# Kernel tuning notes

Measured on AMD Instinct MI355X. Metric: run time of the kernel, lower is better.

The kernel has to match this reference:

```python
import jax, jax.numpy as jnp
import numpy as np

K, D = 2048, 256
B, H, W = 16, 64, 64
DECAY = 0.99
EPS = 1e-05


def setup_inputs() -> dict:
    key = jax.random.key(0)
    k1, k2, k3 = jax.random.split(key, 3)
    z_e = jax.random.normal(k1, (B, D, H, W), dtype=jnp.float32)
    codebook = jax.random.normal(k2, (K, D), dtype=jnp.float32)
    ema_count = jnp.zeros((K,), dtype=jnp.float32)
    ema_weight = jax.random.normal(k3, (K, D), dtype=jnp.float32)
    return {"z_e": z_e, "codebook": codebook, "ema_count": ema_count, "ema_weight": ema_weight}


def reference(z_e, codebook, ema_count, ema_weight):
    b, d, h, w = z_e.shape
    k = codebook.shape[0]
    # [B, D, H, W] -> [B*H*W, D]
    flat = jnp.transpose(z_e, (0, 2, 3, 1)).reshape(-1, d)
    # squared euclidean distances to each code: [N, K]
    dist = (jnp.sum(flat * flat, axis=1, keepdims=True)
            - 2.0 * (flat @ codebook.T)
            + jnp.sum(codebook * codebook, axis=1))
    idx = jnp.argmin(dist, axis=1)  # [N] int
    # gather nearest codes -> [B, D, H, W]
    z_q = jnp.transpose(codebook[idx].reshape(b, h, w, d), (0, 3, 1, 2))
    # EMA statistics (training path, no_grad in torch)
    n = jax.ops.segment_sum(jnp.ones_like(idx, dtype=flat.dtype), idx, num_segments=k)  # [K]
    dw = jax.ops.segment_sum(flat, idx, num_segments=k)  # [K, D]
    new_ema_count = ema_count * DECAY + (1.0 - DECAY) * n
    new_ema_weight = ema_weight * DECAY + (1.0 - DECAY) * dw
    new_codebook = new_ema_weight / (new_ema_count + EPS)[:, None]
    # commitment loss and straight-through estimator
    loss_commit = jnp.mean(jnp.square(z_e - z_q))
    z_q_st = z_e + jax.lax.stop_gradient(z_q - z_e)
    return (z_q_st, idx.reshape(b, h, w), loss_commit,
            new_codebook, new_ema_count, new_ema_weight)
```

## Files before the change

kernel.cpp:

```cpp
#include <hip/hip_runtime.h>
#include <hip/hip_bf16.h>


#define KC 2048
#define DD 256
#define NB 16
#define HWS 4096
#define NPTS 65536
#define DECAYF 0.99f
#define ONEMD 0.01f
#define EPSF 1e-5f
#define NCH 2
#define MARGIN 0.0625f
#define CHPTS 64
#define FPT 64
#define NLOSS 4096

typedef __attribute__((ext_vector_type(8))) short short8v;
typedef __attribute__((ext_vector_type(16))) float f32x16;

#define WS_IDX     0
#define WS_SORTED  262144
#define WS_CNTI    524288
#define WS_START   532480
#define WS_CURSOR  540672
#define WS_FLAGCNT 548864
#define WS_FLAGS   549120
#define WS_LOSSP   549120
#define WS_CNORM   811264
#define WS_PART    819456
#define WS_CBH     5013760
#define WS_CBL     6062336
#define WS_ZH      7110912
#define WS_ZL      40665344
#define WS_NEED_MFMA 74219776ULL
#define WS_NEED_MID  5013760ULL

#define OUT_ZQ   0
#define OUT_IDX  16777216
#define OUT_LOSS (OUT_IDX + NPTS)
#define OUT_CB   (OUT_LOSS + 1)
#define OUT_CNT  (OUT_CB + KC*DD)
#define OUT_W    (OUT_CNT + KC)

static __device__ __forceinline__ unsigned short f2bf_rn(float x) {
    unsigned u = __builtin_bit_cast(unsigned, x);
    unsigned r = (u + 0x7FFFu + ((u >> 16) & 1u)) >> 16;
    return (unsigned short)r;
}
static __device__ __forceinline__ float bf2f(unsigned short h) {
    unsigned u = ((unsigned)h) << 16;
    return __builtin_bit_cast(float, u);
}
static __device__ __forceinline__ void gload_lds16(const unsigned short* g,
                                                   unsigned short* l) {
    __builtin_amdgcn_global_load_lds(
        (const __attribute__((address_space(1))) void*)g,
        (__attribute__((address_space(3))) void*)l, 16, 0, 0);
}

__global__ __launch_bounds__(256) void cbsplit_kernel(const float* __restrict__ cb,
                                                      float* __restrict__ cnorm,
                                                      unsigned short* __restrict__ cbs_h,
                                                      unsigned short* __restrict__ cbs_l) {
    int k = blockIdx.x * 256 + threadIdx.x;
    if (k >= KC) return;
    const int ct = k >> 5, lc = k & 31;
    const float4* row = reinterpret_cast<const float4*>(cb + (size_t)k * DD);
    float s = 0.f;
    #pragma unroll 4
    for (int chunk = 0; chunk < 32; ++chunk) {
        float4 v0 = row[chunk * 2], v1 = row[chunk * 2 + 1];
        float v[8] = {v0.x, v0.y, v0.z, v0.w, v1.x, v1.y, v1.z, v1.w};
        unsigned short hh[8], ll[8];
        #pragma unroll
        for (int j = 0; j < 8; ++j) {
            s += v[j] * v[j];
            hh[j] = f2bf_rn(v[j]);
            ll[j] = f2bf_rn(v[j] - bf2f(hh[j]));
        }
        const int ks = chunk >> 1, h = chunk & 1;
        size_t dst = (size_t)ct * 8192 + ks * 512 + (h * 32 + lc) * 8;
        *reinterpret_cast<ushort4*>(cbs_h + dst)     = *(ushort4*)&hh[0];
        *reinterpret_cast<ushort4*>(cbs_h + dst + 4) = *(ushort4*)&hh[4];
        *reinterpret_cast<ushort4*>(cbs_l + dst)     = *(ushort4*)&ll[0];
        *reinterpret_cast<ushort4*>(cbs_l + dst + 4) = *(ushort4*)&ll[4];
    }
    cnorm[k] = s;
}

__global__ __launch_bounds__(256) void cnorm_kernel(const float* __restrict__ cb,
                                                    float* __restrict__ cnorm) {
    int k = blockIdx.x * 256 + threadIdx.x;
    if (k < KC) {
        const float4* row = reinterpret_cast<const float4*>(cb + (size_t)k * DD);
        float s = 0.f;
        #pragma unroll 8
        for (int i = 0; i < DD / 4; ++i) {
            float4 v = row[i];
            s += v.x * v.x + v.y * v.y + v.z * v.z + v.w * v.w;
        }
        cnorm[k] = s;
    }
}

__global__ __launch_bounds__(256) void transpose_split_kernel(const float* __restrict__ z_e,
                                                              unsigned short* __restrict__ zh,
                                                              unsigned short* __restrict__ zl) {
    __shared__ float t_lds[64][65];
    const int tid = threadIdx.x;
    const int hw0 = blockIdx.x * 64;
    const int d0 = blockIdx.y * 64;
    const int b = blockIdx.z;
    const float* src = z_e + (size_t)b * DD * HWS;
    #pragma unroll
    for (int i = 0; i < 16; ++i) {
        int li = tid + i * 256;
        int d = li >> 6, hw = li & 63;
        t_lds[d][hw] = src[(size_t)(d0 + d) * HWS + hw0 + hw];
    }
    __syncthreads();
    #pragma unroll
    for (int i = 0; i < 16; ++i) {
        int li = tid + i * 256;
        int p = li >> 6, d = li & 63;
        float x = t_lds[d][p];
        unsigned short h = f2bf_rn(x);
        unsigned short l = f2bf_rn(x - bf2f(h));
        size_t o = ((size_t)b * HWS + hw0 + p) * DD + d0 + d;
        zh[o] = h; zl[o] = l;
    }
}

__global__ __launch_bounds__(256, 2) void argmin_mfma_kernel(const unsigned short* __restrict__ zh,
                                                             const unsigned short* __restrict__ zl,
                                                             const unsigned short* __restrict__ cbs_h,
                                                             const unsigned short* __restrict__ cbs_l,
                                                             const float* __restrict__ cnorm,
                                                             int* __restrict__ idx_out,
                                                             int* __restrict__ flagcnt,
                                                             int* __restrict__ flaglist) {
    __shared__ unsigned short lds_cb[2][2][16][512];

    const int tid = threadIdx.x;
    const int w = tid >> 6, lane = tid & 63;
    const int lc = lane & 31, h = lane >> 5;
    const int p = blockIdx.x * 128 + w * 32 + lc;

    const short8v* zhp = reinterpret_cast<const short8v*>(zh + (size_t)p * DD + h * 8);
    const short8v* zlp = reinterpret_cast<const short8v*>(zl + (size_t)p * DD + h * 8);
    short8v bh[16], bl[16];
    #pragma unroll
    for (int ks = 0; ks < 16; ++ks) { bh[ks] = zhp[ks * 2]; bl[ks] = zlp[ks * 2]; }

    auto stage = [&](int ct, int buf) {
        #pragma unroll
        for (int j = 0; j < 8; ++j) {
            const int inst = w * 8 + j;
            const int part = inst >> 4;
            const int ks = inst & 15;
            const unsigned short* src =
                (part ? cbs_l : cbs_h) + (size_t)ct * 8192 + ks * 512 + lane * 8;
            gload_lds16(src, &lds_cb[buf][part][ks][0]);
        }
    };

    float bv1 = 3.4e38f, bv2 = 3.4e38f;
    int bi1 = 0;
    int cur = 0;

    stage(0, 0);
    __syncthreads();

    for (int ct = 0; ct < KC / 32; ++ct) {
        if (ct + 1 < KC / 32) stage(ct + 1, cur ^ 1);

        f32x16 a0, a1, a2;
        #pragma unroll
        for (int i = 0; i < 16; ++i) { a0[i] = 0.f; a1[i] = 0.f; a2[i] = 0.f; }
        #pragma unroll
        for (int ks = 0; ks < 16; ++ks) {
            short8v ah = *reinterpret_cast<const short8v*>(&lds_cb[cur][0][ks][lane * 8]);
            short8v al = *reinterpret_cast<const short8v*>(&lds_cb[cur][1][ks][lane * 8]);
            a0 = __builtin_amdgcn_mfma_f32_32x32x16_bf16(ah, bh[ks], a0, 0, 0, 0);
            a1 = __builtin_amdgcn_mfma_f32_32x32x16_bf16(ah, bl[ks], a1, 0, 0, 0);
            a2 = __builtin_amdgcn_mfma_f32_32x32x16_bf16(al, bh[ks], a2, 0, 0, 0);
        }
        const float* cnb = cnorm + ct * 32 + h * 4;
        #pragma unroll
        for (int g = 0; g < 4; ++g) {
            float4 cn = *reinterpret_cast<const float4*>(cnb + g * 8);
            float cna[4] = {cn.x, cn.y, cn.z, cn.w};
            #pragma unroll
            for (int q = 0; q < 4; ++q) {
                float dot = a0[g * 4 + q] + a1[g * 4 + q] + a2[g * 4 + q];
                float v = fmaf(dot, -2.0f, cna[q]);
                int k = ct * 32 + g * 8 + h * 4 + q;
                bool lt = v < bv1;
                bv2 = fminf(bv2, fmaxf(v, bv1));
                bv1 = fminf(bv1, v);
                bi1 = lt ? k : bi1;
            }
        }
        __syncthreads();
        cur ^= 1;
    }

    float ov1 = __shfl_xor(bv1, 32, 64);
    float ov2 = __shfl_xor(bv2, 32, 64);
    int   oi1 = __shfl_xor(bi1, 32, 64);
    float nv1 = fminf(bv1, ov1);
    float nv2 = fminf(fmaxf(bv1, ov1), fminf(bv2, ov2));
    int ni1 = (ov1 < bv1 || (ov1 == bv1 && oi1 < bi1)) ? oi1 : bi1;

    if (h == 0) {
        idx_out[p] = ni1;
        if (nv2 - nv1 < MARGIN) {
            int pos = atomicAdd(flagcnt, 1);
            flaglist[pos] = p;
        }
    }
}

__global__ __launch_bounds__(256) void fixup_part_kernel(const float* __restrict__ z_e,
                                                         const float* __restrict__ cb,
                                                         const float* __restrict__ cnorm,
                                                         const int* __restrict__ flagcnt,
                                                         const int* __restrict__ flaglist,
                                                         unsigned long long* __restrict__ fixmin) {
    __shared__ float As[64][FPT + 4];
    __shared__ float Bs[64][64 + 4];
    __shared__ float rv[FPT][16];
    __shared__ int   ri[FPT][16];
    __shared__ int   zo[FPT];

    const int tid = threadIdx.x;
    const int tx = tid & 15, ty = tid >> 4;
    const int tot = *flagcnt;
    const int base = blockIdx.x * FPT;
    if (base >= tot) return;
    const int cnt = min(FPT, tot - base);
    const int kt = blockIdx.y * 64;

    if (tid < FPT) {
        int n = flaglist[base + ((tid < cnt) ? tid : 0)];
        zo[tid] = (n >> 12) * DD * HWS + (n & 4095);
    }
    __syncthreads();

    float acc[4][4] = {};
    for (int dc = 0; dc < DD; dc += 64) {
        #pragma unroll
        for (int i = 0; i < 16; ++i) {
            int li = tid + i * 256;
            int d = li >> 6, pp = li & 63;
            As[d][pp] = z_e[(size_t)zo[pp] + (size_t)(dc + d) * HWS];
        }
        #pragma unroll
        for (int i = 0; i < 16; ++i) {
            int li = tid + i * 256;
            int k = li >> 6, d = li & 63;
            Bs[d][k] = cb[(size_t)(kt + k) * DD + dc + d];
        }
        __syncthreads();
        #pragma unroll
        for (int d = 0; d < 64; ++d) {
            const float4 a4 = *reinterpret_cast<const float4*>(&As[d][ty * 4]);
            const float4 b4 = *reinterpret_cast<const float4*>(&Bs[d][tx * 4]);
            const float a[4] = {a4.x, a4.y, a4.z, a4.w};
            const float bb[4] = {b4.x, b4.y, b4.z, b4.w};
            #pragma unroll
            for (int j = 0; j < 4; ++j)
                #pragma unroll
                for (int i = 0; i < 4; ++i)
                    acc[j][i] = fmaf(a[j], bb[i], acc[j][i]);
        }
        __syncthreads();
    }

    float bestv[4]; int besti[4];
    #pragma unroll
    for (int j = 0; j < 4; ++j) { bestv[j] = 3.4e38f; besti[j] = 0; }
    #pragma unroll
    for (int i = 0; i < 4; ++i) {
        int k = kt + tx * 4 + i;
        float c = cnorm[k];
        #pragma unroll
        for (int j = 0; j < 4; ++j) {
            float dist = c - 2.0f * acc[j][i];
            if (dist < bestv[j]) { bestv[j] = dist; besti[j] = k; }
        }
    }
    #pragma unroll
    for (int j = 0; j < 4; ++j) { rv[ty * 4 + j][tx] = bestv[j]; ri[ty * 4 + j][tx] = besti[j]; }
    __syncthreads();

    if (tid < cnt) {
        float bv = rv[tid][0]; int bi = ri[tid][0];
        #pragma unroll
        for (int t = 1; t < 16; ++t) {
            float v = rv[tid][t]; int i2 = ri[tid][t];
            if (v < bv || (v == bv && i2 < bi)) { bv = v; bi = i2; }
        }
        unsigned uv = __float_as_uint(bv);
        uv = (uv & 0x80000000u) ? ~uv : (uv | 0x80000000u);
        unsigned long long key = ((unsigned long long)uv << 32) | (unsigned)bi;
        atomicMin(&fixmin[base + tid], key);
    }
}

__global__ __launch_bounds__(256) void fixup_apply_kernel(const int* __restrict__ flagcnt,
                                                          const int* __restrict__ flaglist,
                                                          const unsigned long long* __restrict__ fixmin,
                                                          int* __restrict__ idx_out) {
    int f = blockIdx.x * 256 + threadIdx.x;
    if (f < *flagcnt)
        idx_out[flaglist[f]] = (int)(fixmin[f] & 0xFFFFFFFFull);
}

#define PT 64
#define KT 64
#define DC 64
__global__ __launch_bounds__(256) void argmin_kernel(const float* __restrict__ z_e,
                                                     const float* __restrict__ cb,
                                                     const float* __restrict__ cnorm,
                                                     int* __restrict__ idx_out) {
    __shared__ float As[DC][PT + 4];
    __shared__ float Bs[DC][KT + 4];
    __shared__ float rv[PT][16];
    __shared__ int   ri[PT][16];
    const int tid = threadIdx.x;
    const int tx = tid & 15, ty = tid >> 4;
    const int n0 = blockIdx.x * PT;
    const int b = n0 >> 12;
    const int hw0 = n0 & 4095;
    const float* zb = z_e + (size_t)b * DD * HWS + hw0;
    float bestv[4]; int besti[4];
    #pragma unroll
    for (int j = 0; j < 4; ++j) { bestv[j] = 3.4e38f; besti[j] = 0; }
    for (int kt = 0; kt < KC; kt += KT) {
        float acc[4][4] = {};
        for (int dc = 0; dc < DD; dc += DC) {
            #pragma unroll
            for (int i = 0; i < 16; ++i) {
                int li = tid + i * 256;
                int d = li >> 6, pp = li & 63;
                As[d][pp] = zb[(size_t)(dc + d) * HWS + pp];
            }
            #pragma unroll
            for (int i = 0; i < 16; ++i) {
                int li = tid + i * 256;
                int k = li >> 6, d = li & 63;
                Bs[d][k] = cb[(size_t)(kt + k) * DD + dc + d];
            }
            __syncthreads();
            #pragma unroll
            for (int d = 0; d < DC; ++d) {
                const float4 a4 = *reinterpret_cast<const float4*>(&As[d][ty * 4]);
                const float4 b4 = *reinterpret_cast<const float4*>(&Bs[d][tx * 4]);
                const float a[4] = {a4.x, a4.y, a4.z, a4.w};
                const float bb[4] = {b4.x, b4.y, b4.z, b4.w};
                #pragma unroll
                for (int j = 0; j < 4; ++j)
                    #pragma unroll
                    for (int i = 0; i < 4; ++i)
                        acc[j][i] = fmaf(a[j], bb[i], acc[j][i]);
            }
            __syncthreads();
        }
        #pragma unroll
        for (int i = 0; i < 4; ++i) {
            int k = kt + tx * 4 + i;
            float c = cnorm[k];
            #pragma unroll
            for (int j = 0; j < 4; ++j) {
                float dist = c - 2.0f * acc[j][i];
                if (dist < bestv[j]) { bestv[j] = dist; besti[j] = k; }
            }
        }
    }
    #pragma unroll
    for (int j = 0; j < 4; ++j) { rv[ty * 4 + j][tx] = bestv[j]; ri[ty * 4 + j][tx] = besti[j]; }
    __syncthreads();
    if (tid < PT) {
        float bv = rv[tid][0]; int bi = ri[tid][0];
        #pragma unroll
        for (int t = 1; t < 16; ++t) {
            float v = rv[tid][t]; int i2 = ri[tid][t];
            if (v < bv || (v == bv && i2 < bi)) { bv = v; bi = i2; }
        }
        idx_out[n0 + tid] = bi;
    }
}

__global__ __launch_bounds__(256) void hist_kernel(const int* __restrict__ idx,
                                                   int* __restrict__ cnti) {
    int n = blockIdx.x * 256 + threadIdx.x;
    atomicAdd(&cnti[idx[n]], 1);
}

__global__ __launch_bounds__(256) void scan_kernel(const int* __restrict__ cnt,
                                                   int* __restrict__ start,
                                                   int* __restrict__ cursor) {
    __shared__ int ps[256];
    const int t = threadIdx.x;
    int v[8], s = 0;
    #pragma unroll
    for (int j = 0; j < 8; ++j) { v[j] = cnt[t * 8 + j]; s += v[j]; }
    ps[t] = s;
    __syncthreads();
    for (int off = 1; off < 256; off <<= 1) {
        int x = (t >= off) ? ps[t - off] : 0;
        __syncthreads();
        ps[t] += x;
        __syncthreads();
    }
    int base = ps[t] - s;
    #pragma unroll
    for (int j = 0; j < 8; ++j) { start[t * 8 + j] = base; cursor[t * 8 + j] = base; base += v[j]; }
}

__global__ __launch_bounds__(256) void scatter_ids_kernel(const int* __restrict__ idx,
                                                          int* __restrict__ cursor,
                                                          int* __restrict__ sorted,
                                                          float* __restrict__ out_idxf) {
    int n = blockIdx.x * 256 + threadIdx.x;
    int k = idx[n];
    out_idxf[n] = (float)k;
    int pos = atomicAdd(&cursor[k], 1);
    sorted[pos] = n;
}

__global__ __launch_bounds__(256) void dw_chunk_kernel(const unsigned short* __restrict__ zh,
                                                       const unsigned short* __restrict__ zl,
                                                       const int* __restrict__ sorted,
                                                       const int* __restrict__ idx,
                                                       float* __restrict__ dwacc) {
    const int t = threadIdx.x;
    const int base = blockIdx.x * CHPTS;
    int kcur = idx[sorted[base]];
    float acc = 0.f;
    for (int i = 0; i < CHPTS; ++i) {
        const int n = sorted[base + i];
        const int k = idx[n];
        if (k != kcur) {
            atomicAdd(&dwacc[(size_t)kcur * DD + t], acc);
            acc = 0.f; kcur = k;
        }
        acc += bf2f(zh[(size_t)n * DD + t]) + bf2f(zl[(size_t)n * DD + t]);
    }
    atomicAdd(&dwacc[(size_t)kcur * DD + t], acc);
}

__global__ __launch_bounds__(256) void dw_direct_kernel(const float* __restrict__ z_e,
                                                        const int* __restrict__ sorted,
                                                        const int* __restrict__ start,
                                                        const int* __restrict__ cnti,
                                                        float* __restrict__ part) {
    const int k = blockIdx.x, c = blockIdx.y, t = threadIdx.x;
    const int s0 = start[k], cnt = cnti[k];
    float acc = 0.f;
    for (int p = c; p < cnt; p += NCH) {
        int n = sorted[s0 + p];
        int b = n >> 12, hw = n & 4095;
        acc += z_e[(size_t)b * DD * HWS + (size_t)t * HWS + hw];
    }
    part[((size_t)k * NCH + c) * DD + t] = acc;
}

__global__ __launch_bounds__(256) void zq_loss_kernel(const float* __restrict__ z_e,
                                                      const float* __restrict__ cb,
                                                      const int* __restrict__ idx,
                                                      float* __restrict__ out_zq,
                                                      float* __restrict__ lossp) {
    const int tid = threadIdx.x;
    const size_t base = ((size_t)blockIdx.x * 256 + tid) * 16;
    const int hw = (int)(base & 4095);
    const int d = (int)((base >> 12) & 255);
    const int b = (int)(base >> 20);
    const int n0 = b * HWS + hw;

    const int4* ip = reinterpret_cast<const int4*>(idx + n0);
    const float4* zp = reinterpret_cast<const float4*>(z_e + base);
    float4* op = reinterpret_cast<float4*>(out_zq + base);

    float ls = 0.f;
    #pragma unroll
    for (int g = 0; g < 4; ++g) {
        int4 i4 = ip[g];
        float4 z4 = zp[g];
        int kk[4] = {i4.x, i4.y, i4.z, i4.w};
        float zz[4] = {z4.x, z4.y, z4.z, z4.w};
        float o4[4];
        #pragma unroll
        for (int q = 0; q < 4; ++q) {
            float qv = cb[(size_t)kk[q] * DD + d];
            o4[q] = zz[q] + (qv - zz[q]);
            float df = zz[q] - qv;
            ls += df * df;
        }
        float4 w4; w4.x = o4[0]; w4.y = o4[1]; w4.z = o4[2]; w4.w = o4[3];
        op[g] = w4;
    }

    #pragma unroll
    for (int off = 32; off > 0; off >>= 1) ls += __shfl_down(ls, off, 64);
    __shared__ float wsum[4];
    if ((tid & 63) == 0) wsum[tid >> 6] = ls;
    __syncthreads();
    if (tid == 0) lossp[blockIdx.x] = wsum[0] + wsum[1] + wsum[2] + wsum[3];
}

__global__ __launch_bounds__(256) void finalize_dw_kernel(const float* __restrict__ ema_count,
                                                          const float* __restrict__ ema_weight,
                                                          const int* __restrict__ cnti,
                                                          const float* __restrict__ dwacc,
                                                          const float* __restrict__ lossp,
                                                          float* __restrict__ out_cb,
                                                          float* __restrict__ out_cnt,
                                                          float* __restrict__ out_w,
                                                          float* __restrict__ out_loss) {
    const int t = blockIdx.x * 256 + threadIdx.x;
    const int k = t >> 8, d = t & 255;
    const float nc = ema_count[k] * DECAYF + ONEMD * (float)cnti[k];
    const float nw = ema_weight[t] * DECAYF + ONEMD * dwacc[t];
    out_w[t] = nw;
    out_cb[t] = nw / (nc + EPSF);
    if (d == 0) out_cnt[k] = nc;

    if (blockIdx.x == 0) {
        __shared__ double sd[256];
        const int tid = threadIdx.x;
        double s = 0.0;
        for (int i = tid; i < NLOSS; i += 256) s += (double)lossp[i];
        sd[tid] = s;
        __syncthreads();
        for (int off = 128; off > 0; off >>= 1) {
            if (tid < off) sd[tid] += sd[tid + off];
            __syncthreads();
        }
        if (tid == 0) out_loss[0] = (float)(sd[0] / 16777216.0);
    }
}

__global__ __launch_bounds__(256) void finalize_part_kernel(const float* __restrict__ ema_count,
                                                            const float* __restrict__ ema_weight,
                                                            const int* __restrict__ cnti,
                                                            const float* __restrict__ part,
                                                            const float* __restrict__ lossp,
                                                            float* __restrict__ out_cb,
                                                            float* __restrict__ out_cnt,
                                                            float* __restrict__ out_w,
                                                            float* __restrict__ out_loss) {
    const int t = blockIdx.x * 256 + threadIdx.x;
    const int k = t >> 8, d = t & 255;
    float dw = 0.f;
    #pragma unroll
    for (int c = 0; c < NCH; ++c) dw += part[((size_t)k * NCH + c) * DD + d];
    const float nc = ema_count[k] * DECAYF + ONEMD * (float)cnti[k];
    const float nw = ema_weight[t] * DECAYF + ONEMD * dw;
    out_w[t] = nw;
    out_cb[t] = nw / (nc + EPSF);
    if (d == 0) out_cnt[k] = nc;

    if (blockIdx.x == 0) {
        __shared__ double sd[256];
        const int tid = threadIdx.x;
        double s = 0.0;
        for (int i = tid; i < NLOSS; i += 256) s += (double)lossp[i];
        sd[tid] = s;
        __syncthreads();
        for (int off = 128; off > 0; off >>= 1) {
            if (tid < off) sd[tid] += sd[tid + off];
            __syncthreads();
        }
        if (tid == 0) out_loss[0] = (float)(sd[0] / 16777216.0);
    }
}

extern "C" void kernel_launch(void* const* d_in, const int* in_sizes, int n_in,
                              void* d_out, int out_size, void* d_ws, size_t ws_size,
                              hipStream_t stream) {
    const float* z_e       = (const float*)d_in[0];
    const float* codebook  = (const float*)d_in[1];
    const float* ema_count = (const float*)d_in[2];
    const float* ema_weight= (const float*)d_in[3];
    float* out = (float*)d_out;
    char* ws = (char*)d_ws;

    int*   ws_idx    = (int*)(ws + WS_IDX);
    int*   ws_sorted = (int*)(ws + WS_SORTED);
    int*   ws_cnti   = (int*)(ws + WS_CNTI);
    int*   ws_start  = (int*)(ws + WS_START);
    int*   ws_cursor = (int*)(ws + WS_CURSOR);
    int*   ws_flagc  = (int*)(ws + WS_FLAGCNT);
    int*   ws_flags  = (int*)(ws + WS_FLAGS);
    float* ws_lossp  = (float*)(ws + WS_LOSSP);
    float* ws_cnorm  = (float*)(ws + WS_CNORM);
    unsigned long long* ws_fixmin = (unsigned long long*)(ws + WS_PART);
    float* ws_dwacc  = (float*)(ws + WS_PART);
    float* ws_part   = (float*)(ws + WS_PART);
    unsigned short* ws_cbh = (unsigned short*)(ws + WS_CBH);
    unsigned short* ws_cbl = (unsigned short*)(ws + WS_CBL);
    unsigned short* ws_zh  = (unsigned short*)(ws + WS_ZH);
    unsigned short* ws_zl  = (unsigned short*)(ws + WS_ZL);

    const bool mfma_path = (ws_size >= WS_NEED_MFMA);
    const bool mid_path  = (ws_size >= WS_NEED_MID);

    hipMemsetAsync(ws + WS_CNTI, 0, (size_t)(WS_FLAGCNT + 256 - WS_CNTI), stream);

    if (mfma_path) {
        hipMemsetAsync(ws + WS_PART, 0xFF, (size_t)NPTS * 8, stream);
        cbsplit_kernel<<<(KC + 255) / 256, 256, 0, stream>>>(codebook, ws_cnorm, ws_cbh, ws_cbl);
        transpose_split_kernel<<<dim3(HWS / 64, DD / 64, NB), 256, 0, stream>>>(z_e, ws_zh, ws_zl);
        argmin_mfma_kernel<<<NPTS / 128, 256, 0, stream>>>(ws_zh, ws_zl, ws_cbh, ws_cbl,
                                                           ws_cnorm, ws_idx, ws_flagc, ws_flags);
        fixup_part_kernel<<<dim3(NPTS / FPT, KC / 64), 256, 0, stream>>>(z_e, codebook, ws_cnorm,
                                                                         ws_flagc, ws_flags,
                                                                         ws_fixmin);
        fixup_apply_kernel<<<NPTS / 256, 256, 0, stream>>>(ws_flagc, ws_flags, ws_fixmin, ws_idx);
        zq_loss_kernel<<<NLOSS, 256, 0, stream>>>(z_e, codebook, ws_idx,
                                                  out + OUT_ZQ, ws_lossp);
        hist_kernel<<<NPTS / 256, 256, 0, stream>>>(ws_idx, ws_cnti);
        scan_kernel<<<1, 256, 0, stream>>>(ws_cnti, ws_start, ws_cursor);
        scatter_ids_kernel<<<NPTS / 256, 256, 0, stream>>>(ws_idx, ws_cursor, ws_sorted,
                                                           out + OUT_IDX);
        hipMemsetAsync(ws + WS_PART, 0, (size_t)KC * DD * 4, stream);
        dw_chunk_kernel<<<NPTS / CHPTS, 256, 0, stream>>>(ws_zh, ws_zl, ws_sorted,
                                                          ws_idx, ws_dwacc);
        finalize_dw_kernel<<<(KC * DD) / 256, 256, 0, stream>>>(ema_count, ema_weight,
                                                                ws_cnti, ws_dwacc, ws_lossp,
                                                                out + OUT_CB, out + OUT_CNT,
                                                                out + OUT_W, out + OUT_LOSS);
    } else if (mid_path) {
        cnorm_kernel<<<(KC + 255) / 256, 256, 0, stream>>>(codebook, ws_cnorm);
        argmin_kernel<<<NPTS / PT, 256, 0, stream>>>(z_e, codebook, ws_cnorm, ws_idx);
        zq_loss_kernel<<<NLOSS, 256, 0, stream>>>(z_e, codebook, ws_idx,
                                                  out + OUT_ZQ, ws_lossp);
        hist_kernel<<<NPTS / 256, 256, 0, stream>>>(ws_idx, ws_cnti);
        scan_kernel<<<1, 256, 0, stream>>>(ws_cnti, ws_start, ws_cursor);
        scatter_ids_kernel<<<NPTS / 256, 256, 0, stream>>>(ws_idx, ws_cursor, ws_sorted,
                                                           out + OUT_IDX);
        dw_direct_kernel<<<dim3(KC, NCH), 256, 0, stream>>>(z_e, ws_sorted,
                                                            ws_start, ws_cnti, ws_part + KC * DD);
        finalize_part_kernel<<<(KC * DD) / 256, 256, 0, stream>>>(ema_count, ema_weight,
                                                                  ws_cnti, ws_part + KC * DD,
                                                                  ws_lossp,
                                                                  out + OUT_CB, out + OUT_CNT,
                                                                  out + OUT_W, out + OUT_LOSS);
    }
}
```

Measured before the change: 449.9 us.

## Fuse prep kernels, fold histogram into argmin, replace memsets with in-kernel zeroing

Merges the codebook split and the z_e transpose/split into one prep kernel, which also zeroes the counters. The histogram moves into argmin as atomics, with fixup_apply correcting the counts for reassigned points, and the fixmin and dwacc memsets are folded into existing kernels. CHPTS is halved so the dw chunk kernel launches more blocks. The aim is fewer launches and memsets, at the cost of extra atomics in argmin and the risk of ordering bugs, for example the cursor zeroing that scan may depend on.

```diff
diff --git a/kernel.cpp b/kernel.cpp
--- a/kernel.cpp
+++ b/kernel.cpp
@@ -12,7 +12,7 @@
 #define EPSF 1e-5f
 #define NCH 2
 #define MARGIN 0.0625f
-#define CHPTS 64
+#define CHPTS 32
 #define FPT 64
 #define NLOSS 4096
 
@@ -59,34 +59,67 @@
         (__attribute__((address_space(3))) void*)l, 16, 0, 0);
 }
 
-__global__ __launch_bounds__(256) void cbsplit_kernel(const float* __restrict__ cb,
-                                                      float* __restrict__ cnorm,
-                                                      unsigned short* __restrict__ cbs_h,
-                                                      unsigned short* __restrict__ cbs_l) {
-    int k = blockIdx.x * 256 + threadIdx.x;
-    if (k >= KC) return;
-    const int ct = k >> 5, lc = k & 31;
-    const float4* row = reinterpret_cast<const float4*>(cb + (size_t)k * DD);
-    float s = 0.f;
-    #pragma unroll 4
-    for (int chunk = 0; chunk < 32; ++chunk) {
-        float4 v0 = row[chunk * 2], v1 = row[chunk * 2 + 1];
-        float v[8] = {v0.x, v0.y, v0.z, v0.w, v1.x, v1.y, v1.z, v1.w};
-        unsigned short hh[8], ll[8];
-        #pragma unroll
-        for (int j = 0; j < 8; ++j) {
-            s += v[j] * v[j];
-            hh[j] = f2bf_rn(v[j]);
-            ll[j] = f2bf_rn(v[j] - bf2f(hh[j]));
-        }
-        const int ks = chunk >> 1, h = chunk & 1;
-        size_t dst = (size_t)ct * 8192 + ks * 512 + (h * 32 + lc) * 8;
-        *reinterpret_cast<ushort4*>(cbs_h + dst)     = *(ushort4*)&hh[0];
-        *reinterpret_cast<ushort4*>(cbs_h + dst + 4) = *(ushort4*)&hh[4];
-        *reinterpret_cast<ushort4*>(cbs_l + dst)     = *(ushort4*)&ll[0];
-        *reinterpret_cast<ushort4*>(cbs_l + dst + 4) = *(ushort4*)&ll[4];
-    }
-    cnorm[k] = s;
+__global__ __launch_bounds__(256) void prep_kernel(const float* __restrict__ z_e,
+                                                   const float* __restrict__ cb,
+                                                   float* __restrict__ cnorm,
+                                                   unsigned short* __restrict__ cbs_h,
+                                                   unsigned short* __restrict__ cbs_l,
+                                                   unsigned short* __restrict__ zh,
+                                                   unsigned short* __restrict__ zl,
+                                                   int* __restrict__ cnti,
+                                                   int* __restrict__ flagcnt) {
+    const int tid = threadIdx.x;
+    if (blockIdx.x >= 4096) {
+        int k = (blockIdx.x - 4096) * 256 + tid;
+        cnti[k] = 0;
+        if (k == 0) *flagcnt = 0;
+        const int ct = k >> 5, lc = k & 31;
+        const float4* row = reinterpret_cast<const float4*>(cb + (size_t)k * DD);
+        float s = 0.f;
+        #pragma unroll 4
+        for (int chunk = 0; chunk < 32; ++chunk) {
+            float4 v0 = row[chunk * 2], v1 = row[chunk * 2 + 1];
+            float v[8] = {v0.x, v0.y, v0.z, v0.w, v1.x, v1.y, v1.z, v1.w};
+            unsigned short hh[8], ll[8];
+            #pragma unroll
+            for (int j = 0; j < 8; ++j) {
+                s += v[j] * v[j];
+                hh[j] = f2bf_rn(v[j]);
+                ll[j] = f2bf_rn(v[j] - bf2f(hh[j]));
+            }
+            const int ks = chunk >> 1, h = chunk & 1;
+            size_t dst = (size_t)ct * 8192 + ks * 512 + (h * 32 + lc) * 8;
+            *reinterpret_cast<ushort4*>(cbs_h + dst)     = *(ushort4*)&hh[0];
+            *reinterpret_cast<ushort4*>(cbs_h + dst + 4) = *(ushort4*)&hh[4];
+            *reinterpret_cast<ushort4*>(cbs_l + dst)     = *(ushort4*)&ll[0];
+            *reinterpret_cast<ushort4*>(cbs_l + dst + 4) = *(ushort4*)&ll[4];
+        }
+        cnorm[k] = s;
+        return;
+    }
+    __shared__ float t_lds[64][65];
+    const int bid = blockIdx.x;
+    const int hw0 = (bid & 63) * 64;
+    const int d0 = ((bid >> 6) & 3) * 64;
+    const int b = bid >> 8;
+    const float* src = z_e + (size_t)b * DD * HWS;
+    #pragma unroll
+    for (int i = 0; i < 16; ++i) {
+        int li = tid + i * 256;
+        int d = li >> 6, hw = li & 63;
+        t_lds[d][hw] = src[(size_t)(d0 + d) * HWS + hw0 + hw];
+    }
+    __syncthreads();
+    #pragma unroll
+    for (int i = 0; i < 16; ++i) {
+        int li = tid + i * 256;
+        int p = li >> 6, d = li & 63;
+        float x = t_lds[d][p];
+        unsigned short h = f2bf_rn(x);
+        unsigned short l = f2bf_rn(x - bf2f(h));
+        size_t o = ((size_t)b * HWS + hw0 + p) * DD + d0 + d;
+        zh[o] = h; zl[o] = l;
+    }
 }
 
 __global__ __launch_bounds__(256) void cnorm_kernel(const float* __restrict__ cb,
@@ -104,42 +137,16 @@
     }
 }
 
-__global__ __launch_bounds__(256) void transpose_split_kernel(const float* __restrict__ z_e,
-                                                              unsigned short* __restrict__ zh,
-                                                              unsigned short* __restrict__ zl) {
-    __shared__ float t_lds[64][65];
-    const int tid = threadIdx.x;
-    const int hw0 = blockIdx.x * 64;
-    const int d0 = blockIdx.y * 64;
-    const int b = blockIdx.z;
-    const float* src = z_e + (size_t)b * DD * HWS;
-    #pragma unroll
-    for (int i = 0; i < 16; ++i) {
-        int li = tid + i * 256;
-        int d = li >> 6, hw = li & 63;
-        t_lds[d][hw] = src[(size_t)(d0 + d) * HWS + hw0 + hw];
-    }
-    __syncthreads();
-    #pragma unroll
-    for (int i = 0; i < 16; ++i) {
-        int li = tid + i * 256;
-        int p = li >> 6, d = li & 63;
-        float x = t_lds[d][p];
-        unsigned short h = f2bf_rn(x);
-        unsigned short l = f2bf_rn(x - bf2f(h));
-        size_t o = ((size_t)b * HWS + hw0 + p) * DD + d0 + d;
-        zh[o] = h; zl[o] = l;
-    }
-}
-
 __global__ __launch_bounds__(256, 2) void argmin_mfma_kernel(const unsigned short* __restrict__ zh,
                                                              const unsigned short* __restrict__ zl,
                                                              const unsigned short* __restrict__ cbs_h,
                                                              const unsigned short* __restrict__ cbs_l,
                                                              const float* __restrict__ cnorm,
                                                              int* __restrict__ idx_out,
+                                                             int* __restrict__ cnti,
                                                              int* __restrict__ flagcnt,
-                                                             int* __restrict__ flaglist) {
+                                                             int* __restrict__ flaglist,
+                                                             unsigned long long* __restrict__ fixmin) {
     __shared__ unsigned short lds_cb[2][2][16][512];
 
     const int tid = threadIdx.x;
@@ -215,9 +222,11 @@
 
     if (h == 0) {
         idx_out[p] = ni1;
+        atomicAdd(&cnti[ni1], 1);
         if (nv2 - nv1 < MARGIN) {
             int pos = atomicAdd(flagcnt, 1);
             flaglist[pos] = p;
+            fixmin[pos] = ~0ULL;
         }
     }
 }
@@ -312,10 +321,19 @@
 __global__ __launch_bounds__(256) void fixup_apply_kernel(const int* __restrict__ flagcnt,
                                                           const int* __restrict__ flaglist,
                                                           const unsigned long long* __restrict__ fixmin,
-                                                          int* __restrict__ idx_out) {
+                                                          int* __restrict__ idx_out,
+                                                          int* __restrict__ cnti) {
     int f = blockIdx.x * 256 + threadIdx.x;
-    if (f < *flagcnt)
-        idx_out[flaglist[f]] = (int)(fixmin[f] & 0xFFFFFFFFull);
+    if (f < *flagcnt) {
+        int n = flaglist[f];
+        int nk = (int)(fixmin[f] & 0xFFFFFFFFull);
+        int ok = idx_out[n];
+        if (nk != ok) {
+            atomicSub(&cnti[ok], 1);
+            atomicAdd(&cnti[nk], 1);
+            idx_out[n] = nk;
+        }
+    }
 }
 
 #define PT 64
@@ -423,12 +441,16 @@
 __global__ __launch_bounds__(256) void scatter_ids_kernel(const int* __restrict__ idx,
                                                           int* __restrict__ cursor,
                                                           int* __restrict__ sorted,
-                                                          float* __restrict__ out_idxf) {
+                                                          float* __restrict__ out_idxf,
+                                                          float* __restrict__ dwacc) {
     int n = blockIdx.x * 256 + threadIdx.x;
     int k = idx[n];
     out_idxf[n] = (float)k;
     int pos = atomicAdd(&cursor[k], 1);
     sorted[pos] = n;
+    #pragma unroll
+    for (int i = 0; i < (KC * DD) / NPTS; ++i)
+        dwacc[n + i * NPTS] = 0.f;
 }
 
 __global__ __launch_bounds__(256) void dw_chunk_kernel(const unsigned short* __restrict__ zh,
@@ -608,25 +630,22 @@
     const bool mfma_path = (ws_size >= WS_NEED_MFMA);
     const bool mid_path  = (ws_size >= WS_NEED_MID);
 
-    hipMemsetAsync(ws + WS_CNTI, 0, (size_t)(WS_FLAGCNT + 256 - WS_CNTI), stream);
-
     if (mfma_path) {
-        hipMemsetAsync(ws + WS_PART, 0xFF, (size_t)NPTS * 8, stream);
-        cbsplit_kernel<<<(KC + 255) / 256, 256, 0, stream>>>(codebook, ws_cnorm, ws_cbh, ws_cbl);
-        transpose_split_kernel<<<dim3(HWS / 64, DD / 64, NB), 256, 0, stream>>>(z_e, ws_zh, ws_zl);
+        prep_kernel<<<4104, 256, 0, stream>>>(z_e, codebook, ws_cnorm, ws_cbh, ws_cbl,
+                                              ws_zh, ws_zl, ws_cnti, ws_flagc);
         argmin_mfma_kernel<<<NPTS / 128, 256, 0, stream>>>(ws_zh, ws_zl, ws_cbh, ws_cbl,
-                                                           ws_cnorm, ws_idx, ws_flagc, ws_flags);
+                                                           ws_cnorm, ws_idx, ws_cnti,
+                                                           ws_flagc, ws_flags, ws_fixmin);
         fixup_part_kernel<<<dim3(NPTS / FPT, KC / 64), 256, 0, stream>>>(z_e, codebook, ws_cnorm,
                                                                          ws_flagc, ws_flags,
                                                                          ws_fixmin);
-        fixup_apply_kernel<<<NPTS / 256, 256, 0, stream>>>(ws_flagc, ws_flags, ws_fixmin, ws_idx);
+        fixup_apply_kernel<<<NPTS / 256, 256, 0, stream>>>(ws_flagc, ws_flags, ws_fixmin,
+                                                           ws_idx, ws_cnti);
         zq_loss_kernel<<<NLOSS, 256, 0, stream>>>(z_e, codebook, ws_idx,
                                                   out + OUT_ZQ, ws_lossp);
-        hist_kernel<<<NPTS / 256, 256, 0, stream>>>(ws_idx, ws_cnti);
         scan_kernel<<<1, 256, 0, stream>>>(ws_cnti, ws_start, ws_cursor);
         scatter_ids_kernel<<<NPTS / 256, 256, 0, stream>>>(ws_idx, ws_cursor, ws_sorted,
-                                                           out + OUT_IDX);
-        hipMemsetAsync(ws + WS_PART, 0, (size_t)KC * DD * 4, stream);
+                                                           out + OUT_IDX, ws_dwacc);
         dw_chunk_kernel<<<NPTS / CHPTS, 256, 0, stream>>>(ws_zh, ws_zl, ws_sorted,
                                                           ws_idx, ws_dwacc);
         finalize_dw_kernel<<<(KC * DD) / 256, 256, 0, stream>>>(ema_count, ema_weight,
@@ -634,6 +653,7 @@
                                                                 out + OUT_CB, out + OUT_CNT,
                                                                 out + OUT_W, out + OUT_LOSS);
     } else if (mid_path) {
+        hipMemsetAsync(ws + WS_CNTI, 0, (size_t)(WS_FLAGCNT + 256 - WS_CNTI), stream);
         cnorm_kernel<<<(KC + 255) / 256, 256, 0, stream>>>(codebook, ws_cnorm);
         argmin_kernel<<<NPTS / PT, 256, 0, stream>>>(z_e, codebook, ws_cnorm, ws_idx);
         zq_loss_kernel<<<NLOSS, 256, 0, stream>>>(z_e, codebook, ws_idx,
@@ -641,7 +661,7 @@
         hist_kernel<<<NPTS / 256, 256, 0, stream>>>(ws_idx, ws_cnti);
         scan_kernel<<<1, 256, 0, stream>>>(ws_cnti, ws_start, ws_cursor);
         scatter_ids_kernel<<<NPTS / 256, 256, 0, stream>>>(ws_idx, ws_cursor, ws_sorted,
-                                                           out + OUT_IDX);
+                                                           out + OUT_IDX, ws_part);
         dw_direct_kernel<<<dim3(KC, NCH), 256, 0, stream>>>(z_e, ws_sorted,
                                                             ws_start, ws_cnti, ws_part + KC * DD);
         finalize_part_kernel<<<(KC * DD) / 256, 256, 0, stream>>>(ema_count, ema_weight,
```

New measurement: 409.3 us. -9.0%, faster.
